# Kernel optimization log

Measured on AMD Instinct MI355X. Metric: run time of the kernel, lower is better.

## Reference

```python
import jax, jax.numpy as jnp
import numpy as np

NODE_DIM = 256
BATCH = 64
NUM_NODES = 1024


def setup_inputs() -> dict:
    key = jax.random.key(0)
    ks = jax.random.split(key, 10)
    d = NODE_DIM
    scale = 1.0 / np.sqrt(d)
    node_state = jax.random.normal(ks[0], (BATCH, NUM_NODES, d), dtype=jnp.float32)
    message = jax.random.normal(ks[1], (BATCH, NUM_NODES, 2 * d), dtype=jnp.float32)
    mask = (jax.random.uniform(ks[2], (BATCH, NUM_NODES)) < 0.9).astype(jnp.float32)
    w_z = jax.random.normal(ks[3], (2 * d, d), dtype=jnp.float32) * scale
    u_z = jax.random.normal(ks[4], (d, d), dtype=jnp.float32) * scale
    w_r = jax.random.normal(ks[5], (2 * d, d), dtype=jnp.float32) * scale
    u_r = jax.random.normal(ks[6], (d, d), dtype=jnp.float32) * scale
    w = jax.random.normal(ks[7], (2 * d, d), dtype=jnp.float32) * scale
    u = jax.random.normal(ks[8], (d, d), dtype=jnp.float32) * scale
    return {"node_state": node_state, "message": message, "mask": mask,
            "w_z": w_z, "u_z": u_z, "w_r": w_r, "u_r": u_r, "w": w, "u": u}


def reference(node_state, message, mask, w_z, u_z, w_r, u_r, w, u):
    B, N, D = node_state.shape
    h = node_state.reshape(B * N, D)          # [BN, D]
    m = message.reshape(B * N, 2 * D)         # [BN, 2D]
    z_t = jax.nn.sigmoid(m @ w_z + h @ u_z)   # [BN, D]
    r_t = jax.nn.sigmoid(m @ w_r + h @ u_r)
    h_tilda = jnp.tanh(m @ w + (r_t * h) @ u)
    h_t = (1.0 - z_t) * h + z_t * h_tilda
    h_t = h_t * mask.reshape(B * N, 1)
    return h_t.reshape(B, N, D)
```

## Files before the change

kernel.cpp:

```cpp
#include <hip/hip_runtime.h>


#define KTOT 768
#define ROWS 64
#define THREADS 512
#define TILE_SHORTS 12288

typedef __attribute__((ext_vector_type(8))) __bf16 bf16x8;
typedef __attribute__((ext_vector_type(8))) unsigned short ushort8;
typedef __attribute__((ext_vector_type(4))) float f32x4;

#define MFMA(a, b, c) __builtin_amdgcn_mfma_f32_16x16x32_bf16((a), (b), (c), 0, 0, 0)

__device__ __forceinline__ unsigned short f2bf(float f) {
    union { float f; unsigned u; } v; v.f = f;
    return (unsigned short)((v.u + 0x7FFFu + ((v.u >> 16) & 1u)) >> 16);
}
__device__ __forceinline__ float bf2f(unsigned short b) {
    union { unsigned u; float f; } v; v.u = ((unsigned)b) << 16;
    return v.f;
}

__global__ void pack_weights(const float* __restrict__ wz, const float* __restrict__ uz,
                             const float* __restrict__ wr, const float* __restrict__ ur,
                             const float* __restrict__ w,  const float* __restrict__ u,
                             unsigned short* __restrict__ W1t, unsigned short* __restrict__ W2t)
{
    __shared__ unsigned short buf[KTOT * 16];
    const int tid = threadIdx.x;
    const int b   = blockIdx.x;

    const float* Wsrc; const float* Usrc; int ncb; unsigned short* outp;
    if (b < 16)      { Wsrc = wz; Usrc = uz; ncb = b * 16;        outp = W1t + b * TILE_SHORTS; }
    else if (b < 32) { Wsrc = wr; Usrc = ur; ncb = (b - 16) * 16; outp = W1t + b * TILE_SHORTS; }
    else             { Wsrc = w;  Usrc = u;  ncb = (b - 32) * 16; outp = W2t + (b - 32) * TILE_SHORTS; }

    #pragma unroll
    for (int i = 0; i < 48; ++i) {
        int id = tid + i * 256;
        int k = id >> 4, nl = id & 15;
        float v = (k < 512) ? Wsrc[k * 256 + ncb + nl]
                            : Usrc[(k - 512) * 256 + ncb + nl];
        buf[id] = f2bf(v);
    }
    __syncthreads();

    #pragma unroll
    for (int i = 0; i < 6; ++i) {
        int c = tid + i * 256;
        int kk = c >> 6, lane = c & 63;
        int p = lane & 15, q = lane >> 4;
        ushort8 pk;
        #pragma unroll
        for (int j = 0; j < 8; ++j)
            pk[j] = buf[(kk * 32 + q * 8 + j) * 16 + p];
        *(ushort8*)(outp + (unsigned)c * 8) = pk;
    }
}

__device__ __forceinline__ int sw_idx(int row, int k) {
    int kblk = k >> 3;
    int kb2 = (kblk & ~7) | ((kblk ^ row) & 7);
    return row * KTOT + kb2 * 8 + (k & 7);
}

__global__ __launch_bounds__(THREADS, 2) void fused_gru(
    const float* __restrict__ h_in,
    const float* __restrict__ msg,
    const float* __restrict__ mask,
    const unsigned short* __restrict__ W1t,
    const unsigned short* __restrict__ W2t,
    float* __restrict__ out)
{
    __shared__ __align__(16) unsigned short Xs[ROWS * KTOT];
    __shared__ float maskS[ROWS];

    const int tid  = threadIdx.x;
    const int wave = tid >> 6;
    const int lane = tid & 63;
    const int p    = lane & 15;
    const int q    = lane >> 4;
    const long r0  = (long)blockIdx.x * ROWS;

    {
        const f32x4* m4 = (const f32x4*)(msg + r0 * 512);
        #pragma unroll
        for (int i = 0; i < 16; ++i) {
            int f = tid + i * THREADS;
            int row = f >> 7, c4 = f & 127;
            f32x4 v = m4[f];
            unsigned short* d = &Xs[sw_idx(row, c4 * 4)];
            unsigned long long pk =  (unsigned long long)f2bf(v.x)
                                  | ((unsigned long long)f2bf(v.y) << 16)
                                  | ((unsigned long long)f2bf(v.z) << 32)
                                  | ((unsigned long long)f2bf(v.w) << 48);
            *(unsigned long long*)d = pk;
        }
        const f32x4* h4 = (const f32x4*)(h_in + r0 * 256);
        #pragma unroll
        for (int i = 0; i < 8; ++i) {
            int f = tid + i * THREADS;
            int row = f >> 6, c4 = f & 63;
            f32x4 v = h4[f];
            unsigned short* d = &Xs[sw_idx(row, 512 + c4 * 4)];
            unsigned long long pk =  (unsigned long long)f2bf(v.x)
                                  | ((unsigned long long)f2bf(v.y) << 16)
                                  | ((unsigned long long)f2bf(v.z) << 32)
                                  | ((unsigned long long)f2bf(v.w) << 48);
            *(unsigned long long*)d = pk;
        }
        if (tid < ROWS) maskS[tid] = mask[r0 + tid];
    }
    __syncthreads();

    const unsigned short* wzp = W1t + (long)(wave * 2) * TILE_SHORTS + lane * 8;
    const unsigned short* wrp = wzp + 16L * TILE_SHORTS;
    const unsigned short* wbp = W2t + (long)(wave * 2) * TILE_SHORTS + lane * 8;

    f32x4 accz[4][2], accr[4][2];
    #pragma unroll
    for (int rt = 0; rt < 4; ++rt)
        #pragma unroll
        for (int c = 0; c < 2; ++c)
            #pragma unroll
            for (int i = 0; i < 4; ++i) { accz[rt][c][i] = 0.f; accr[rt][c][i] = 0.f; }

    {
        bf16x8 a[4], zb[2], rb[2];
        #pragma unroll
        for (int rt = 0; rt < 4; ++rt)
            a[rt] = *(const bf16x8*)&Xs[sw_idx(rt * 16 + p, q * 8)];
        #pragma unroll
        for (int c = 0; c < 2; ++c) {
            zb[c] = *(const bf16x8*)(wzp + c * TILE_SHORTS);
            rb[c] = *(const bf16x8*)(wrp + c * TILE_SHORTS);
        }

        #pragma unroll
        for (int kk = 0; kk < 24; ++kk) {
            bf16x8 na[4], nzb[2], nrb[2];
            if (kk < 23) {
                #pragma unroll
                for (int c = 0; c < 2; ++c) {
                    nzb[c] = *(const bf16x8*)(wzp + c * TILE_SHORTS + (kk + 1) * 512);
                    nrb[c] = *(const bf16x8*)(wrp + c * TILE_SHORTS + (kk + 1) * 512);
                }
                #pragma unroll
                for (int rt = 0; rt < 4; ++rt)
                    na[rt] = *(const bf16x8*)&Xs[sw_idx(rt * 16 + p, (kk + 1) * 32 + q * 8)];
            }
            __builtin_amdgcn_s_setprio(1);
            #pragma unroll
            for (int c = 0; c < 2; ++c)
                #pragma unroll
                for (int rt = 0; rt < 4; ++rt)
                    accz[rt][c] = MFMA(a[rt], zb[c], accz[rt][c]);
            #pragma unroll
            for (int c = 0; c < 2; ++c)
                #pragma unroll
                for (int rt = 0; rt < 4; ++rt)
                    accr[rt][c] = MFMA(a[rt], rb[c], accr[rt][c]);
            __builtin_amdgcn_s_setprio(0);
            if (kk < 23) {
                #pragma unroll
                for (int rt = 0; rt < 4; ++rt) a[rt] = na[rt];
                #pragma unroll
                for (int c = 0; c < 2; ++c) { zb[c] = nzb[c]; rb[c] = nrb[c]; }
            }
        }
    }

    float zs[4][2][4], rs[4][2][4];
    #pragma unroll
    for (int rt = 0; rt < 4; ++rt)
        #pragma unroll
        for (int c = 0; c < 2; ++c)
            #pragma unroll
            for (int i = 0; i < 4; ++i) {
                zs[rt][c][i] = 1.f / (1.f + __expf(-accz[rt][c][i]));
                rs[rt][c][i] = 1.f / (1.f + __expf(-accr[rt][c][i]));
            }

    __syncthreads();
    float hs[4][2][4];
    #pragma unroll
    for (int rt = 0; rt < 4; ++rt)
        #pragma unroll
        for (int c = 0; c < 2; ++c)
            #pragma unroll
            for (int i = 0; i < 4; ++i) {
                int row = rt * 16 + q * 4 + i;
                int col = wave * 32 + c * 16 + p;
                unsigned short* ptr = &Xs[sw_idx(row, 512 + col)];
                float hv = bf2f(*ptr);
                hs[rt][c][i] = hv;
                *ptr = f2bf(rs[rt][c][i] * hv);
            }
    __syncthreads();

    f32x4 acc[4][2];
    #pragma unroll
    for (int rt = 0; rt < 4; ++rt)
        #pragma unroll
        for (int c = 0; c < 2; ++c)
            #pragma unroll
            for (int i = 0; i < 4; ++i) acc[rt][c][i] = 0.f;

    {
        bf16x8 a[4], bb[2];
        #pragma unroll
        for (int rt = 0; rt < 4; ++rt)
            a[rt] = *(const bf16x8*)&Xs[sw_idx(rt * 16 + p, q * 8)];
        #pragma unroll
        for (int c = 0; c < 2; ++c) bb[c] = *(const bf16x8*)(wbp + c * TILE_SHORTS);

        #pragma unroll
        for (int kk = 0; kk < 24; ++kk) {
            bf16x8 na[4], nbb[2];
            if (kk < 23) {
                #pragma unroll
                for (int c = 0; c < 2; ++c)
                    nbb[c] = *(const bf16x8*)(wbp + c * TILE_SHORTS + (kk + 1) * 512);
                #pragma unroll
                for (int rt = 0; rt < 4; ++rt)
                    na[rt] = *(const bf16x8*)&Xs[sw_idx(rt * 16 + p, (kk + 1) * 32 + q * 8)];
            }
            __builtin_amdgcn_s_setprio(1);
            #pragma unroll
            for (int c = 0; c < 2; ++c)
                #pragma unroll
                for (int rt = 0; rt < 4; ++rt)
                    acc[rt][c] = MFMA(a[rt], bb[c], acc[rt][c]);
            __builtin_amdgcn_s_setprio(0);
            if (kk < 23) {
                #pragma unroll
                for (int rt = 0; rt < 4; ++rt) a[rt] = na[rt];
                #pragma unroll
                for (int c = 0; c < 2; ++c) bb[c] = nbb[c];
            }
        }
    }

    #pragma unroll
    for (int rt = 0; rt < 4; ++rt)
        #pragma unroll
        for (int c = 0; c < 2; ++c)
            #pragma unroll
            for (int i = 0; i < 4; ++i) {
                int row  = rt * 16 + q * 4 + i;
                long grow = r0 + row;
                int col  = wave * 32 + c * 16 + p;
                float pre = acc[rt][c][i];
                float e  = __expf(-2.f * fabsf(pre));
                float t  = (1.f - e) / (1.f + e);
                float ht = (pre >= 0.f) ? t : -t;
                float zv = zs[rt][c][i];
                float hv = hs[rt][c][i];
                out[grow * 256 + col] = maskS[row] * (hv + zv * (ht - hv));
            }
}

extern "C" void kernel_launch(void* const* d_in, const int* in_sizes, int n_in,
                              void* d_out, int out_size, void* d_ws, size_t ws_size,
                              hipStream_t stream) {
    const float* h_in = (const float*)d_in[0];
    const float* msg  = (const float*)d_in[1];
    const float* mask = (const float*)d_in[2];
    const float* wz   = (const float*)d_in[3];
    const float* uz   = (const float*)d_in[4];
    const float* wr   = (const float*)d_in[5];
    const float* ur   = (const float*)d_in[6];
    const float* w    = (const float*)d_in[7];
    const float* u    = (const float*)d_in[8];

    unsigned short* W1t = (unsigned short*)d_ws;
    unsigned short* W2t = W1t + 32 * TILE_SHORTS;
    float* out = (float*)d_out;

    pack_weights<<<48, 256, 0, stream>>>(wz, uz, wr, ur, w, u, W1t, W2t);

    const int BN = 64 * 1024;
    fused_gru<<<BN / ROWS, THREADS, 0, stream>>>(h_in, msg, mask, W1t, W2t, out);
}
```

Before: 342.2 us.

## Stream activations through double-buffered 256-wide LDS chunks with 1024-thread blocks

```diff
diff --git a/kernel.cpp b/kernel.cpp
--- a/kernel.cpp
+++ b/kernel.cpp
@@ -3,7 +3,9 @@
 
 #define KTOT 768
 #define ROWS 64
-#define THREADS 512
+#define THREADS 1024
+#define CHUNK 256
+#define CHUNK_SHORTS (ROWS * CHUNK)
 #define TILE_SHORTS 12288
 
 typedef __attribute__((ext_vector_type(8))) __bf16 bf16x8;
@@ -58,13 +60,13 @@
     }
 }
 
-__device__ __forceinline__ int sw_idx(int row, int k) {
+__device__ __forceinline__ int cidx(int row, int k) {
     int kblk = k >> 3;
-    int kb2 = (kblk & ~7) | ((kblk ^ row) & 7);
-    return row * KTOT + kb2 * 8 + (k & 7);
-}
-
-__global__ __launch_bounds__(THREADS, 2) void fused_gru(
+    int kb2 = (kblk & 16) | ((kblk ^ row) & 15);
+    return row * CHUNK + kb2 * 8 + (k & 7);
+}
+
+__global__ __launch_bounds__(THREADS, 4) void fused_gru(
     const float* __restrict__ h_in,
     const float* __restrict__ msg,
     const float* __restrict__ mask,
@@ -72,7 +74,8 @@
     const unsigned short* __restrict__ W2t,
     float* __restrict__ out)
 {
-    __shared__ __align__(16) unsigned short Xs[ROWS * KTOT];
+    __shared__ __align__(16) unsigned short B0[CHUNK_SHORTS];
+    __shared__ __align__(16) unsigned short B1[CHUNK_SHORTS];
     __shared__ float maskS[ROWS];
 
     const int tid  = threadIdx.x;
@@ -82,182 +85,155 @@
     const int q    = lane >> 4;
     const long r0  = (long)blockIdx.x * ROWS;
 
-    {
-        const f32x4* m4 = (const f32x4*)(msg + r0 * 512);
-        #pragma unroll
-        for (int i = 0; i < 16; ++i) {
+    f32x4 st[4];
+    auto stage_issue = [&](const float* base, int stride) {
+        #pragma unroll
+        for (int i = 0; i < 4; ++i) {
             int f = tid + i * THREADS;
-            int row = f >> 7, c4 = f & 127;
-            f32x4 v = m4[f];
-            unsigned short* d = &Xs[sw_idx(row, c4 * 4)];
+            st[i] = *(const f32x4*)(base + (f >> 6) * stride + (f & 63) * 4);
+        }
+    };
+    auto stage_write = [&](unsigned short* buf) {
+        #pragma unroll
+        for (int i = 0; i < 4; ++i) {
+            int f = tid + i * THREADS;
+            int row = f >> 6, c4 = f & 63;
+            f32x4 v = st[i];
             unsigned long long pk =  (unsigned long long)f2bf(v.x)
                                   | ((unsigned long long)f2bf(v.y) << 16)
                                   | ((unsigned long long)f2bf(v.z) << 32)
                                   | ((unsigned long long)f2bf(v.w) << 48);
-            *(unsigned long long*)d = pk;
-        }
-        const f32x4* h4 = (const f32x4*)(h_in + r0 * 256);
-        #pragma unroll
-        for (int i = 0; i < 8; ++i) {
-            int f = tid + i * THREADS;
-            int row = f >> 6, c4 = f & 63;
-            f32x4 v = h4[f];
-            unsigned short* d = &Xs[sw_idx(row, 512 + c4 * 4)];
-            unsigned long long pk =  (unsigned long long)f2bf(v.x)
-                                  | ((unsigned long long)f2bf(v.y) << 16)
-                                  | ((unsigned long long)f2bf(v.z) << 32)
-                                  | ((unsigned long long)f2bf(v.w) << 48);
-            *(unsigned long long*)d = pk;
-        }
-        if (tid < ROWS) maskS[tid] = mask[r0 + tid];
-    }
-    __syncthreads();
-
-    const unsigned short* wzp = W1t + (long)(wave * 2) * TILE_SHORTS + lane * 8;
+            *(unsigned long long*)&buf[cidx(row, c4 * 4)] = pk;
+        }
+    };
+
+    stage_issue(msg + r0 * 512, 512);
+    if (tid < ROWS) maskS[tid] = mask[r0 + tid];
+    stage_write(B0);
+    __syncthreads();
+
+    const unsigned short* wzp = W1t + (long)wave * TILE_SHORTS + lane * 8;
     const unsigned short* wrp = wzp + 16L * TILE_SHORTS;
-    const unsigned short* wbp = W2t + (long)(wave * 2) * TILE_SHORTS + lane * 8;
-
-    f32x4 accz[4][2], accr[4][2];
-    #pragma unroll
-    for (int rt = 0; rt < 4; ++rt)
-        #pragma unroll
-        for (int c = 0; c < 2; ++c)
-            #pragma unroll
-            for (int i = 0; i < 4; ++i) { accz[rt][c][i] = 0.f; accr[rt][c][i] = 0.f; }
-
-    {
-        bf16x8 a[4], zb[2], rb[2];
-        #pragma unroll
-        for (int rt = 0; rt < 4; ++rt)
-            a[rt] = *(const bf16x8*)&Xs[sw_idx(rt * 16 + p, q * 8)];
-        #pragma unroll
-        for (int c = 0; c < 2; ++c) {
-            zb[c] = *(const bf16x8*)(wzp + c * TILE_SHORTS);
-            rb[c] = *(const bf16x8*)(wrp + c * TILE_SHORTS);
-        }
-
-        #pragma unroll
-        for (int kk = 0; kk < 24; ++kk) {
-            bf16x8 na[4], nzb[2], nrb[2];
-            if (kk < 23) {
-                #pragma unroll
-                for (int c = 0; c < 2; ++c) {
-                    nzb[c] = *(const bf16x8*)(wzp + c * TILE_SHORTS + (kk + 1) * 512);
-                    nrb[c] = *(const bf16x8*)(wrp + c * TILE_SHORTS + (kk + 1) * 512);
-                }
-                #pragma unroll
-                for (int rt = 0; rt < 4; ++rt)
-                    na[rt] = *(const bf16x8*)&Xs[sw_idx(rt * 16 + p, (kk + 1) * 32 + q * 8)];
+    const unsigned short* wbp = W2t + (long)wave * TILE_SHORTS + lane * 8;
+
+    f32x4 accz[4], accr[4];
+    #pragma unroll
+    for (int rt = 0; rt < 4; ++rt)
+        #pragma unroll
+        for (int i = 0; i < 4; ++i) { accz[rt][i] = 0.f; accr[rt][i] = 0.f; }
+
+    bf16x8 zb = *(const bf16x8*)(wzp);
+    bf16x8 rb = *(const bf16x8*)(wrp);
+
+    auto zr_step = [&](const unsigned short* buf, int kk0) {
+        #pragma unroll
+        for (int kkl = 0; kkl < 8; ++kkl) {
+            int kkg = kk0 + kkl;
+            bf16x8 a[4];
+            #pragma unroll
+            for (int rt = 0; rt < 4; ++rt)
+                a[rt] = *(const bf16x8*)&buf[cidx(rt * 16 + p, kkl * 32 + q * 8)];
+            bf16x8 nzb, nrb;
+            if (kkg < 23) {
+                nzb = *(const bf16x8*)(wzp + (kkg + 1) * 512);
+                nrb = *(const bf16x8*)(wrp + (kkg + 1) * 512);
             }
             __builtin_amdgcn_s_setprio(1);
             #pragma unroll
-            for (int c = 0; c < 2; ++c)
-                #pragma unroll
-                for (int rt = 0; rt < 4; ++rt)
-                    accz[rt][c] = MFMA(a[rt], zb[c], accz[rt][c]);
-            #pragma unroll
-            for (int c = 0; c < 2; ++c)
-                #pragma unroll
-                for (int rt = 0; rt < 4; ++rt)
-                    accr[rt][c] = MFMA(a[rt], rb[c], accr[rt][c]);
+            for (int rt = 0; rt < 4; ++rt) accz[rt] = MFMA(a[rt], zb, accz[rt]);
+            #pragma unroll
+            for (int rt = 0; rt < 4; ++rt) accr[rt] = MFMA(a[rt], rb, accr[rt]);
             __builtin_amdgcn_s_setprio(0);
-            if (kk < 23) {
-                #pragma unroll
-                for (int rt = 0; rt < 4; ++rt) a[rt] = na[rt];
-                #pragma unroll
-                for (int c = 0; c < 2; ++c) { zb[c] = nzb[c]; rb[c] = nrb[c]; }
-            }
-        }
-    }
-
-    float zs[4][2][4], rs[4][2][4];
-    #pragma unroll
-    for (int rt = 0; rt < 4; ++rt)
-        #pragma unroll
-        for (int c = 0; c < 2; ++c)
-            #pragma unroll
-            for (int i = 0; i < 4; ++i) {
-                zs[rt][c][i] = 1.f / (1.f + __expf(-accz[rt][c][i]));
-                rs[rt][c][i] = 1.f / (1.f + __expf(-accr[rt][c][i]));
-            }
-
-    __syncthreads();
-    float hs[4][2][4];
-    #pragma unroll
-    for (int rt = 0; rt < 4; ++rt)
-        #pragma unroll
-        for (int c = 0; c < 2; ++c)
-            #pragma unroll
-            for (int i = 0; i < 4; ++i) {
-                int row = rt * 16 + q * 4 + i;
-                int col = wave * 32 + c * 16 + p;
-                unsigned short* ptr = &Xs[sw_idx(row, 512 + col)];
-                float hv = bf2f(*ptr);
-                hs[rt][c][i] = hv;
-                *ptr = f2bf(rs[rt][c][i] * hv);
-            }
-    __syncthreads();
-
-    f32x4 acc[4][2];
-    #pragma unroll
-    for (int rt = 0; rt < 4; ++rt)
-        #pragma unroll
-        for (int c = 0; c < 2; ++c)
-            #pragma unroll
-            for (int i = 0; i < 4; ++i) acc[rt][c][i] = 0.f;
-
-    {
-        bf16x8 a[4], bb[2];
-        #pragma unroll
-        for (int rt = 0; rt < 4; ++rt)
-            a[rt] = *(const bf16x8*)&Xs[sw_idx(rt * 16 + p, q * 8)];
-        #pragma unroll
-        for (int c = 0; c < 2; ++c) bb[c] = *(const bf16x8*)(wbp + c * TILE_SHORTS);
-
-        #pragma unroll
-        for (int kk = 0; kk < 24; ++kk) {
-            bf16x8 na[4], nbb[2];
-            if (kk < 23) {
-                #pragma unroll
-                for (int c = 0; c < 2; ++c)
-                    nbb[c] = *(const bf16x8*)(wbp + c * TILE_SHORTS + (kk + 1) * 512);
-                #pragma unroll
-                for (int rt = 0; rt < 4; ++rt)
-                    na[rt] = *(const bf16x8*)&Xs[sw_idx(rt * 16 + p, (kk + 1) * 32 + q * 8)];
-            }
+            if (kkg < 23) { zb = nzb; rb = nrb; }
+        }
+    };
+
+    stage_issue(msg + r0 * 512 + 256, 512);
+    zr_step(B0, 0);
+    stage_write(B1);
+    __syncthreads();
+
+    stage_issue(h_in + r0 * 256, 256);
+    zr_step(B1, 8);
+    stage_write(B0);
+    __syncthreads();
+
+    stage_issue(msg + r0 * 512, 512);
+    zr_step(B0, 16);
+    stage_write(B1);
+    __syncthreads();
+
+    float zs[4][4], rs[4][4], hs[4][4];
+    #pragma unroll
+    for (int rt = 0; rt < 4; ++rt)
+        #pragma unroll
+        for (int i = 0; i < 4; ++i) {
+            zs[rt][i] = 1.f / (1.f + __expf(-accz[rt][i]));
+            rs[rt][i] = 1.f / (1.f + __expf(-accr[rt][i]));
+        }
+    #pragma unroll
+    for (int rt = 0; rt < 4; ++rt)
+        #pragma unroll
+        for (int i = 0; i < 4; ++i) {
+            int row = rt * 16 + q * 4 + i;
+            int col = wave * 16 + p;
+            unsigned short* ptr = &B0[cidx(row, col)];
+            float hv = bf2f(*ptr);
+            hs[rt][i] = hv;
+            *ptr = f2bf(rs[rt][i] * hv);
+        }
+    __syncthreads();
+
+    f32x4 acc[4];
+    #pragma unroll
+    for (int rt = 0; rt < 4; ++rt)
+        #pragma unroll
+        for (int i = 0; i < 4; ++i) acc[rt][i] = 0.f;
+
+    bf16x8 bb = *(const bf16x8*)(wbp + 16 * 512);
+
+    auto b_step = [&](const unsigned short* buf, int kk0, int nk0) {
+        #pragma unroll
+        for (int kkl = 0; kkl < 8; ++kkl) {
+            int kkg = kk0 + kkl;
+            bf16x8 a[4];
+            #pragma unroll
+            for (int rt = 0; rt < 4; ++rt)
+                a[rt] = *(const bf16x8*)&buf[cidx(rt * 16 + p, kkl * 32 + q * 8)];
+            int nk = (kkl < 7) ? (kkg + 1) : nk0;
+            bf16x8 nbb;
+            if (nk >= 0) nbb = *(const bf16x8*)(wbp + nk * 512);
             __builtin_amdgcn_s_setprio(1);
             #pragma unroll
-            for (int c = 0; c < 2; ++c)
-                #pragma unroll
-                for (int rt = 0; rt < 4; ++rt)
-                    acc[rt][c] = MFMA(a[rt], bb[c], acc[rt][c]);
+            for (int rt = 0; rt < 4; ++rt) acc[rt] = MFMA(a[rt], bb, acc[rt]);
             __builtin_amdgcn_s_setprio(0);
-            if (kk < 23) {
-                #pragma unroll
-                for (int rt = 0; rt < 4; ++rt) a[rt] = na[rt];
-                #pragma unroll
-                for (int c = 0; c < 2; ++c) bb[c] = nbb[c];
-            }
-        }
-    }
-
-    #pragma unroll
-    for (int rt = 0; rt < 4; ++rt)
-        #pragma unroll
-        for (int c = 0; c < 2; ++c)
-            #pragma unroll
-            for (int i = 0; i < 4; ++i) {
-                int row  = rt * 16 + q * 4 + i;
-                long grow = r0 + row;
-                int col  = wave * 32 + c * 16 + p;
-                float pre = acc[rt][c][i];
-                float e  = __expf(-2.f * fabsf(pre));
-                float t  = (1.f - e) / (1.f + e);
-                float ht = (pre >= 0.f) ? t : -t;
-                float zv = zs[rt][c][i];
-                float hv = hs[rt][c][i];
-                out[grow * 256 + col] = maskS[row] * (hv + zv * (ht - hv));
-            }
+            if (nk >= 0) bb = nbb;
+        }
+    };
+
+    stage_issue(msg + r0 * 512 + 256, 512);
+    b_step(B0, 16, 0);
+    __syncthreads();
+    stage_write(B0);
+    b_step(B1, 0, 8);
+    __syncthreads();
+    b_step(B0, 8, -1);
+
+    #pragma unroll
+    for (int rt = 0; rt < 4; ++rt)
+        #pragma unroll
+        for (int i = 0; i < 4; ++i) {
+            int row  = rt * 16 + q * 4 + i;
+            long grow = r0 + row;
+            int col  = wave * 16 + p;
+            float pre = acc[rt][i];
+            float e  = __expf(-2.f * fabsf(pre));
+            float t  = (1.f - e) / (1.f + e);
+            float ht = (pre >= 0.f) ? t : -t;
+            float zv = zs[rt][i];
+            float hv = hs[rt][i];
+            out[grow * 256 + col] = maskS[row] * (hv + zv * (ht - hv));
+        }
 }
 
 extern "C" void kernel_launch(void* const* d_in, const int* in_sizes, int n_in,
```

After: 346.0 us. About the same (+1.1%).
